# Kernel optimization log

Measured on AMD Instinct MI355X. Metric: run time of the kernel, lower is better.

Reference implementation:

```python
import jax, jax.numpy as jnp
import numpy as np

NUM_HEADS = 4

def setup_inputs() -> dict:
    key = jax.random.key(0)
    ks = jax.random.split(key, 8)
    B, C, H, W = 4, 256, 128, 128
    Cq = C // 8  # query/key channels
    x  = jax.random.normal(ks[0], (B, C, H, W), dtype=jnp.float32)
    Wq = jax.random.normal(ks[1], (Cq, C), dtype=jnp.float32) * 0.05
    bq = jax.random.normal(ks[2], (Cq,),  dtype=jnp.float32) * 0.01
    Wk = jax.random.normal(ks[3], (Cq, C), dtype=jnp.float32) * 0.05
    bk = jax.random.normal(ks[4], (Cq,),  dtype=jnp.float32) * 0.01
    Wv = jax.random.normal(ks[5], (C, C),  dtype=jnp.float32) * 0.05
    bv = jax.random.normal(ks[6], (C,),   dtype=jnp.float32) * 0.01
    # torch init is zeros; use a nonzero value so the attention path contributes
    gamma = jnp.array([0.5], dtype=jnp.float32)
    return {"x": x, "Wq": Wq, "bq": bq, "Wk": Wk, "bk": bk, "Wv": Wv, "bv": bv, "gamma": gamma}

def _conv1x1(x, Wm, b):
    # 1x1 conv == per-pixel linear map over channels
    return jnp.einsum('bchw,oc->bohw', x, Wm) + b[None, :, None, None]

def reference(x, Wq, bq, Wk, bk, Wv, bv, gamma):
    B, C, H, W = x.shape
    nh = NUM_HEADS
    # project, then fold heads into batch: (B*nh, c_head, H, W)
    q = _conv1x1(x, Wq, bq).reshape(B * nh, -1, H, W)
    k = _conv1x1(x, Wk, bk).reshape(B * nh, -1, H, W)
    v = _conv1x1(x, Wv, bv).reshape(B * nh, -1, H, W)
    # horizontal (row-wise) attention over W: energy [BH, H, W, W]
    e_h = jnp.einsum('bchw,bchv->bhwv', q, k)
    a_h = jax.nn.softmax(e_h, axis=-1)
    o_h = jnp.einsum('bhwv,bchv->bchw', a_h, v)  # (BH, cv, H, W)
    # vertical (column-wise) attention over H: energy [BH, W, H, H]
    e_v = jnp.einsum('bchw,bcgw->bwhg', q, k)
    a_v = jax.nn.softmax(e_v, axis=-1)
    # original permutes back as (BH, cv, W, H); requires H == W to add
    o_v = jnp.einsum('bwhg,bcgw->bcwh', a_v, v)
    attn = (o_h + o_v).reshape(B, C, H, W)
    return gamma * attn + x
```

## Files before the change

### kernel.cpp

```cpp
#include <hip/hip_runtime.h>

#define HW 16384

typedef __attribute__((ext_vector_type(8))) short short8;
typedef __attribute__((ext_vector_type(16))) float floatx16;

__device__ inline unsigned short f2bf(float f) {
    unsigned u = __builtin_bit_cast(unsigned, f);
    u = (u + 0x7FFFu + ((u >> 16) & 1u)) >> 16;
    return (unsigned short)u;
}

__device__ inline unsigned pack_bf_trunc(float lo, float hi) {
    return __builtin_amdgcn_perm(__builtin_bit_cast(unsigned, hi),
                                 __builtin_bit_cast(unsigned, lo), 0x07060302u);
}

__global__ __launch_bounds__(256) void castW_kernel(
    const float* __restrict__ Wq, const float* __restrict__ Wk,
    const float* __restrict__ Wv, unsigned short* __restrict__ Wb)
{
    int idx4 = blockIdx.x * 256 + threadIdx.x;
    int e0 = idx4 * 4;
    int row = e0 >> 8, col = e0 & 255;
    const float* src = (row < 32) ? (Wq + row * 256 + col)
                     : (row < 64) ? (Wk + (row - 32) * 256 + col)
                                  : (Wv + (row - 64) * 256 + col);
    float4 v = *(const float4*)src;
    uint2 pk;
    pk.x = f2bf(v.x) | ((unsigned)f2bf(v.y) << 16);
    pk.y = f2bf(v.z) | ((unsigned)f2bf(v.w) << 16);
    *(uint2*)&Wb[e0] = pk;
}

__global__ __launch_bounds__(256) void cast_xt_kernel(
    const float* __restrict__ x, unsigned short* __restrict__ xt)
{
    __shared__ unsigned short T[64][66];
    const int tid = threadIdx.x;
    const int p0 = blockIdx.x * 64;
    const int c0 = blockIdx.y * 64;
    const int b  = blockIdx.z;
    #pragma unroll
    for (int i = 0; i < 4; i++) {
        int e = i * 256 + tid;
        int c = e >> 4, seg = e & 15;
        float4 v = *(const float4*)&x[((b * 256 + c0 + c) << 14) + p0 + seg * 4];
        ((unsigned*)&T[c][seg * 4])[0] = f2bf(v.x) | ((unsigned)f2bf(v.y) << 16);
        ((unsigned*)&T[c][seg * 4])[1] = f2bf(v.z) | ((unsigned)f2bf(v.w) << 16);
    }
    __syncthreads();
    #pragma unroll
    for (int i = 0; i < 2; i++) {
        int e = i * 256 + tid;
        int p = e >> 3, cs = e & 7;
        unsigned short t[8];
        #pragma unroll
        for (int j = 0; j < 8; j++) t[j] = T[cs * 8 + j][p];
        uint4 pk;
        pk.x = t[0] | ((unsigned)t[1] << 16);
        pk.y = t[2] | ((unsigned)t[3] << 16);
        pk.z = t[4] | ((unsigned)t[5] << 16);
        pk.w = t[6] | ((unsigned)t[7] << 16);
        *(uint4*)&xt[(((b << 14) + p0 + p) << 8) + c0 + cs * 8] = pk;
    }
}

__global__ __launch_bounds__(256, 3) void proj_mfma_kernel(
    const unsigned short* __restrict__ Wb, const unsigned short* __restrict__ xt,
    const float* __restrict__ bq, const float* __restrict__ bk,
    const float* __restrict__ bv,
    unsigned short* __restrict__ qb, unsigned short* __restrict__ kb,
    unsigned short* __restrict__ vb)
{
    __shared__ __align__(16) unsigned short As[64 * 64];
    __shared__ __align__(16) unsigned short Bs[256 * 64];
    __shared__ float biasS[64];
    const int tid = threadIdx.x;
    const int p0  = blockIdx.x * 256;
    const int oc0 = blockIdx.y * 64;
    const int b   = blockIdx.z;
    const int w = tid >> 6, lr = tid & 31, lh = (tid & 63) >> 5;

    if (tid < 64) biasS[tid] = (oc0 == 0) ? ((tid < 32) ? bq[tid] : bk[tid - 32])
                                          : bv[oc0 - 64 + tid];

    floatx16 z16 = {0,0,0,0,0,0,0,0,0,0,0,0,0,0,0,0};
    floatx16 acc[2][2] = {{z16, z16}, {z16, z16}};
    const int bpx = (b << 14) + p0;

    for (int kc = 0; kc < 256; kc += 64) {
        if (kc) __syncthreads();
        #pragma unroll
        for (int i = 0; i < 2; i++) {
            int e = i * 256 + tid;
            int row = e >> 3, seg = e & 7, cp = seg ^ (row & 7);
            *(uint4*)&As[row * 64 + cp * 8] =
                *(const uint4*)&Wb[(oc0 + row) * 256 + kc + seg * 8];
        }
        #pragma unroll
        for (int i = 0; i < 8; i++) {
            int e = i * 256 + tid;
            int row = e >> 3, seg = e & 7, cp = seg ^ (row & 7);
            *(uint4*)&Bs[row * 64 + cp * 8] =
                *(const uint4*)&xt[((bpx + row) << 8) + kc + seg * 8];
        }
        __syncthreads();
        #pragma unroll
        for (int ks = 0; ks < 4; ks++) {
            int c = 2 * ks + lh;
            int cx = (c ^ (lr & 7)) * 8;
            short8 af0 = *(const short8*)&As[lr * 64 + cx];
            short8 af1 = *(const short8*)&As[(32 + lr) * 64 + cx];
            short8 bf0 = *(const short8*)&Bs[(64 * w + lr) * 64 + cx];
            short8 bf1 = *(const short8*)&Bs[(64 * w + 32 + lr) * 64 + cx];
            acc[0][0] = __builtin_amdgcn_mfma_f32_32x32x16_bf16(af0, bf0, acc[0][0], 0, 0, 0);
            acc[0][1] = __builtin_amdgcn_mfma_f32_32x32x16_bf16(af0, bf1, acc[0][1], 0, 0, 0);
            acc[1][0] = __builtin_amdgcn_mfma_f32_32x32x16_bf16(af1, bf0, acc[1][0], 0, 0, 0);
            acc[1][1] = __builtin_amdgcn_mfma_f32_32x32x16_bf16(af1, bf1, acc[1][1], 0, 0, 0);
        }
    }

    __syncthreads();
    if (oc0 == 0) {
        unsigned short* Cq = Bs;
        #pragma unroll
        for (int i = 0; i < 2; i++) {
            #pragma unroll
            for (int j = 0; j < 2; j++) {
                int px = 64 * w + 32 * j + lr;
                #pragma unroll
                for (int g = 0; g < 4; g++) {
                    float v0 = acc[i][j][4*g+0] + biasS[32*i + 8*g + 4*lh + 0];
                    float v1 = acc[i][j][4*g+1] + biasS[32*i + 8*g + 4*lh + 1];
                    float v2 = acc[i][j][4*g+2] + biasS[32*i + 8*g + 4*lh + 2];
                    float v3 = acc[i][j][4*g+3] + biasS[32*i + 8*g + 4*lh + 3];
                    uint2 u; u.x = pack_bf_trunc(v0, v1); u.y = pack_bf_trunc(v2, v3);
                    int cp = (4 * i + g) ^ (px & 7);
                    *(uint2*)&Cq[px * 64 + cp * 8 + 4 * lh] = u;
                }
            }
        }
        __syncthreads();
        #pragma unroll
        for (int i = 0; i < 8; i++) {
            int px = tid;
            int cp = i ^ (px & 7);
            uint4 val = *(const uint4*)&Cq[px * 64 + cp * 8];
            if (i < 4) *(uint4*)&qb[(unsigned)((b * 4 + i)     * HW + p0 + px) * 8] = val;
            else       *(uint4*)&kb[(unsigned)((b * 4 + i - 4) * HW + p0 + px) * 8] = val;
        }
    } else {
        unsigned short* Cv = Bs;
        #pragma unroll
        for (int i = 0; i < 2; i++) {
            #pragma unroll
            for (int j = 0; j < 2; j++) {
                int px = 64 * w + 32 * j + lr;
                #pragma unroll
                for (int reg = 0; reg < 16; reg++) {
                    int oc = 32 * i + (reg & 3) + 8 * (reg >> 2) + 4 * lh;
                    float v = acc[i][j][reg] + biasS[oc];
                    int cp = (px >> 3) ^ (oc & 31);
                    Cv[oc * 256 + cp * 8 + (px & 7)] =
                        (unsigned short)(__builtin_bit_cast(unsigned, v) >> 16);
                }
            }
        }
        __syncthreads();
        #pragma unroll
        for (int i = 0; i < 8; i++) {
            int u = i * 256 + tid;
            int oc = u >> 5, seg = u & 31;
            int cp = seg ^ (oc & 31);
            uint4 val = *(const uint4*)&Cv[oc * 256 + cp * 8];
            *(uint4*)&vb[(unsigned)(b * 256 + oc0 - 64 + oc) * HW + p0 + seg * 8] = val;
        }
    }
}

__global__ __launch_bounds__(256) void tqk_kernel(
    const unsigned short* __restrict__ qb, const unsigned short* __restrict__ kb,
    unsigned short* __restrict__ qt, unsigned short* __restrict__ kt)
{
    __shared__ uint4 t[32][33];
    const int plane = blockIdx.y;
    const int tile  = blockIdx.x;
    const int tx = tile & 3, ty = tile >> 2;
    const uint4* src = (const uint4*)(plane < 16 ? qb : kb) + (plane & 15) * HW;
    uint4*       dst = (uint4*)(plane < 16 ? qt : kt) + (plane & 15) * HW;
    const int c = threadIdx.x & 31, r0 = threadIdx.x >> 5;
    #pragma unroll
    for (int i = 0; i < 4; i++) {
        int r = r0 + i * 8;
        t[r][c] = src[(ty * 32 + r) * 128 + tx * 32 + c];
    }
    __syncthreads();
    #pragma unroll
    for (int i = 0; i < 4; i++) {
        int r = r0 + i * 8;
        dst[(tx * 32 + r) * 128 + ty * 32 + c] = t[c][r];
    }
}

__global__ __launch_bounds__(256) void tv_kernel(
    const unsigned short* __restrict__ vb, unsigned short* __restrict__ vt)
{
    __shared__ unsigned short T[64][66];
    const int plane = blockIdx.y;
    const int tile  = blockIdx.x;
    const int tx = tile & 1, ty = tile >> 1;
    const unsigned* src = (const unsigned*)(vb + plane * HW);
    unsigned*       dst = (unsigned*)(vt + plane * HW);
    const int tid = threadIdx.x;
    #pragma unroll
    for (int i = 0; i < 8; i++) {
        int e = i * 256 + tid;
        int r = e >> 5, cp = e & 31;
        *(unsigned*)&T[r][2 * cp] = src[(ty * 64 + r) * 64 + tx * 32 + cp];
    }
    __syncthreads();
    #pragma unroll
    for (int i = 0; i < 8; i++) {
        int e = i * 256 + tid;
        int c = e >> 5, rp = e & 31;
        unsigned lo = T[2 * rp][c], hi = T[2 * rp + 1][c];
        dst[(tx * 64 + c) * 64 + ty * 32 + rp] = lo | (hi << 16);
    }
}

__global__ __launch_bounds__(256, 3) void attn_kernel(
    const unsigned short* __restrict__ qb, const unsigned short* __restrict__ kb,
    const unsigned short* __restrict__ vb,
    const unsigned short* __restrict__ qt, const unsigned short* __restrict__ kt,
    const unsigned short* __restrict__ vt,
    const float* __restrict__ xin, const float* __restrict__ gamma,
    float* __restrict__ out)
{
    __shared__ __align__(16) unsigned short Vs[64 * 128];
    __shared__ __align__(16) unsigned short Ps[128 * 128];
    __shared__ float red[4][128];

    const int tid = threadIdx.x;
    const int y = blockIdx.x, bh = blockIdx.y;
    const int w = tid >> 6, l = tid & 63, lr = l & 31, lh = l >> 5;
    const float L2E = 1.4426950408889634f;

    floatx16 z16 = {0,0,0,0,0,0,0,0,0,0,0,0,0,0,0,0};
    floatx16 o0 = z16, o1 = z16;
    short8 z8 = {0,0,0,0,0,0,0,0};

    for (int stage = 0; stage < 2; stage++) {
        const unsigned short* qsrc = (stage ? qt : qb) + (bh * 128 + y) * 1024;
        const unsigned short* ksrc = (stage ? kt : kb) + (bh * 128 + y) * 1024;
        const unsigned short* vsrc = stage ? vt : vb;
        if (stage) __syncthreads();
        #pragma unroll
        for (int i = 0; i < 4; i++) {
            int e = i * 256 + tid;
            int ch = e >> 4, sg = e & 15;
            int sgp = sg ^ (ch & 15);
            *(uint4*)&Vs[ch * 128 + sgp * 8] =
                *(const uint4*)(vsrc + (bh * 64 + ch) * HW + y * 128 + sg * 8);
        }
        short8 af = z8;
        short8 bf[4] = {z8, z8, z8, z8};
        if (lh == 0) {
            af = *(const short8*)(ksrc + (32 * w + lr) * 8);
            #pragma unroll
            for (int nt = 0; nt < 4; nt++)
                bf[nt] = *(const short8*)(qsrc + (32 * nt + lr) * 8);
        }
        floatx16 et[4];
        #pragma unroll
        for (int nt = 0; nt < 4; nt++)
            et[nt] = __builtin_amdgcn_mfma_f32_32x32x16_bf16(af, bf[nt], z16, 0, 0, 0);

        #pragma unroll
        for (int nt = 0; nt < 4; nt++) {
            float s = 0.f;
            #pragma unroll
            for (int r = 0; r < 16; r++) {
                float p = exp2f(et[nt][r] * L2E);
                et[nt][r] = p;
                s += p;
            }
            s += __shfl_xor(s, 32);
            if (lh == 0) red[w][32 * nt + lr] = s;
        }
        __syncthreads();
        float rl[4];
        #pragma unroll
        for (int nt = 0; nt < 4; nt++) {
            int q = 32 * nt + lr;
            rl[nt] = 1.0f / (red[0][q] + red[1][q] + red[2][q] + red[3][q]);
        }
        #pragma unroll
        for (int nt = 0; nt < 4; nt++) {
            int row = 32 * nt + lr;
            #pragma unroll
            for (int g = 0; g < 4; g++) {
                uint2 u;
                u.x = pack_bf_trunc(et[nt][4*g+0] * rl[nt], et[nt][4*g+1] * rl[nt]);
                u.y = pack_bf_trunc(et[nt][4*g+2] * rl[nt], et[nt][4*g+3] * rl[nt]);
                int cp = (4 * w + g) ^ (lr & 15);
                *(uint2*)&Ps[row * 128 + cp * 8 + 4 * lh] = u;
            }
        }
        __syncthreads();
        #pragma unroll
        for (int ks = 0; ks < 8; ks++) {
            int cp = ((2 * ks + lh) ^ (lr & 15)) * 8;
            short8 pf = *(const short8*)&Ps[(32 * w + lr) * 128 + cp];
            short8 v0 = *(const short8*)&Vs[lr * 128 + cp];
            short8 v1 = *(const short8*)&Vs[(32 + lr) * 128 + cp];
            o0 = __builtin_amdgcn_mfma_f32_32x32x16_bf16(v0, pf, o0, 0, 0, 0);
            o1 = __builtin_amdgcn_mfma_f32_32x32x16_bf16(v1, pf, o1, 0, 0, 0);
        }
    }

    const float g = gamma[0];
    const int xq = 32 * w + lr;
    #pragma unroll
    for (int reg = 0; reg < 16; reg++) {
        int ch = (reg & 3) + 8 * (reg >> 2) + 4 * lh;
        int idx0 = (bh * 64 + ch) * HW + y * 128 + xq;
        int idx1 = (bh * 64 + 32 + ch) * HW + y * 128 + xq;
        out[idx0] = g * o0[reg] + xin[idx0];
        out[idx1] = g * o1[reg] + xin[idx1];
    }
}

extern "C" void kernel_launch(void* const* d_in, const int* in_sizes, int n_in,
                              void* d_out, int out_size, void* d_ws, size_t ws_size,
                              hipStream_t stream) {
    const float* x     = (const float*)d_in[0];
    const float* Wq    = (const float*)d_in[1];
    const float* bq    = (const float*)d_in[2];
    const float* Wk    = (const float*)d_in[3];
    const float* bk    = (const float*)d_in[4];
    const float* Wv    = (const float*)d_in[5];
    const float* bv    = (const float*)d_in[6];
    const float* gamma = (const float*)d_in[7];
    float* out = (float*)d_out;

    unsigned short* Wb   = (unsigned short*)d_ws;
    unsigned short* qb16 = Wb + 320 * 256;
    unsigned short* kb16 = qb16 + 16 * HW * 8;
    unsigned short* qt16 = kb16 + 16 * HW * 8;
    unsigned short* kt16 = qt16 + 16 * HW * 8;
    unsigned short* vb16 = kt16 + 16 * HW * 8;
    unsigned short* vt16 = vb16 + 1024 * HW;
    unsigned short* xt = (unsigned short*)d_out;

    castW_kernel<<<dim3(80), 256, 0, stream>>>(Wq, Wk, Wv, Wb);
    cast_xt_kernel<<<dim3(256, 4, 4), 256, 0, stream>>>(x, xt);
    proj_mfma_kernel<<<dim3(64, 5, 4), 256, 0, stream>>>(Wb, xt, bq, bk, bv, qb16, kb16, vb16);
    tqk_kernel<<<dim3(16, 32), 256, 0, stream>>>(qb16, kb16, qt16, kt16);
    tv_kernel<<<dim3(4, 1024), 256, 0, stream>>>(vb16, vt16);
    attn_kernel<<<dim3(128, 16), 256, 0, stream>>>(qb16, kb16, vb16, qt16, kt16, vt16, x, gamma, out);
}
```

Baseline: 202.4 us.

## Keep softmax probabilities in registers and defer normalization to the epilogue

Each wave now computes energy for its own 32 queries across all 128 keys, so the row sums live inside the wave. This removes the cross-wave shared reduction and the Ps staging buffer in shared memory. Probabilities stay unnormalized in registers and are repacked into MFMA B-operand layout with lane shuffles. The stage-0 accumulator is rescaled by the ratio of the two stages' sums, and the final 1/sum is folded into gamma. Both V tiles are loaded once up front into a double shared buffer, and occupancy hint drops from 3 to 2 blocks, trading occupancy for more registers.

Result: no change. 201.2 us (-0.6%).

```diff
diff --git a/kernel.cpp b/kernel.cpp
--- a/kernel.cpp
+++ b/kernel.cpp
@@ -4,6 +4,7 @@
 
 typedef __attribute__((ext_vector_type(8))) short short8;
 typedef __attribute__((ext_vector_type(16))) float floatx16;
+typedef __attribute__((ext_vector_type(4))) unsigned int uvec4;
 
 __device__ inline unsigned short f2bf(float f) {
     unsigned u = __builtin_bit_cast(unsigned, f);
@@ -229,7 +230,7 @@
     }
 }
 
-__global__ __launch_bounds__(256, 3) void attn_kernel(
+__global__ __launch_bounds__(256, 2) void attn_kernel(
     const unsigned short* __restrict__ qb, const unsigned short* __restrict__ kb,
     const unsigned short* __restrict__ vb,
     const unsigned short* __restrict__ qt, const unsigned short* __restrict__ kt,
@@ -237,97 +238,98 @@
     const float* __restrict__ xin, const float* __restrict__ gamma,
     float* __restrict__ out)
 {
-    __shared__ __align__(16) unsigned short Vs[64 * 128];
-    __shared__ __align__(16) unsigned short Ps[128 * 128];
-    __shared__ float red[4][128];
+    __shared__ __align__(16) unsigned short Vs[2][64 * 128];
 
     const int tid = threadIdx.x;
     const int y = blockIdx.x, bh = blockIdx.y;
     const int w = tid >> 6, l = tid & 63, lr = l & 31, lh = l >> 5;
     const float L2E = 1.4426950408889634f;
 
+    #pragma unroll
+    for (int s = 0; s < 2; s++) {
+        const unsigned short* vsrc = s ? vt : vb;
+        #pragma unroll
+        for (int i = 0; i < 4; i++) {
+            int e = i * 256 + tid;
+            int ch = e >> 4, sg = e & 15, sgp = sg ^ (ch & 15);
+            *(uint4*)&Vs[s][ch * 128 + sgp * 8] =
+                *(const uint4*)(vsrc + (bh * 64 + ch) * HW + y * 128 + sg * 8);
+        }
+    }
+    __syncthreads();
+
     floatx16 z16 = {0,0,0,0,0,0,0,0,0,0,0,0,0,0,0,0};
     floatx16 o0 = z16, o1 = z16;
     short8 z8 = {0,0,0,0,0,0,0,0};
-
+    float s0s = 1.0f;
+
+    #pragma unroll
     for (int stage = 0; stage < 2; stage++) {
         const unsigned short* qsrc = (stage ? qt : qb) + (bh * 128 + y) * 1024;
         const unsigned short* ksrc = (stage ? kt : kb) + (bh * 128 + y) * 1024;
-        const unsigned short* vsrc = stage ? vt : vb;
-        if (stage) __syncthreads();
-        #pragma unroll
-        for (int i = 0; i < 4; i++) {
-            int e = i * 256 + tid;
-            int ch = e >> 4, sg = e & 15;
-            int sgp = sg ^ (ch & 15);
-            *(uint4*)&Vs[ch * 128 + sgp * 8] =
-                *(const uint4*)(vsrc + (bh * 64 + ch) * HW + y * 128 + sg * 8);
-        }
-        short8 af = z8;
-        short8 bf[4] = {z8, z8, z8, z8};
-        if (lh == 0) {
-            af = *(const short8*)(ksrc + (32 * w + lr) * 8);
-            #pragma unroll
-            for (int nt = 0; nt < 4; nt++)
-                bf[nt] = *(const short8*)(qsrc + (32 * nt + lr) * 8);
-        }
-        floatx16 et[4];
-        #pragma unroll
-        for (int nt = 0; nt < 4; nt++)
-            et[nt] = __builtin_amdgcn_mfma_f32_32x32x16_bf16(af, bf[nt], z16, 0, 0, 0);
-
-        #pragma unroll
-        for (int nt = 0; nt < 4; nt++) {
-            float s = 0.f;
+        short8 bf = z8;
+        if (lh == 0) bf = *(const short8*)(qsrc + (32 * w + lr) * 8);
+
+        float partial = 0.f;
+        short8 pf[8];
+        #pragma unroll
+        for (int kg = 0; kg < 4; kg++) {
+            short8 af = z8;
+            if (lh == 0) af = *(const short8*)(ksrc + (32 * kg + lr) * 8);
+            floatx16 e = __builtin_amdgcn_mfma_f32_32x32x16_bf16(af, bf, z16, 0, 0, 0);
             #pragma unroll
             for (int r = 0; r < 16; r++) {
-                float p = exp2f(et[nt][r] * L2E);
-                et[nt][r] = p;
-                s += p;
+                float p = exp2f(e[r] * L2E);
+                e[r] = p;
+                partial += p;
             }
-            s += __shfl_xor(s, 32);
-            if (lh == 0) red[w][32 * nt + lr] = s;
-        }
-        __syncthreads();
-        float rl[4];
-        #pragma unroll
-        for (int nt = 0; nt < 4; nt++) {
-            int q = 32 * nt + lr;
-            rl[nt] = 1.0f / (red[0][q] + red[1][q] + red[2][q] + red[3][q]);
-        }
-        #pragma unroll
-        for (int nt = 0; nt < 4; nt++) {
-            int row = 32 * nt + lr;
-            #pragma unroll
-            for (int g = 0; g < 4; g++) {
-                uint2 u;
-                u.x = pack_bf_trunc(et[nt][4*g+0] * rl[nt], et[nt][4*g+1] * rl[nt]);
-                u.y = pack_bf_trunc(et[nt][4*g+2] * rl[nt], et[nt][4*g+3] * rl[nt]);
-                int cp = (4 * w + g) ^ (lr & 15);
-                *(uint2*)&Ps[row * 128 + cp * 8 + 4 * lh] = u;
+            #pragma unroll
+            for (int cc = 0; cc < 2; cc++) {
+                unsigned X0 = pack_bf_trunc(e[8*cc+0], e[8*cc+1]);
+                unsigned X1 = pack_bf_trunc(e[8*cc+2], e[8*cc+3]);
+                unsigned X2 = pack_bf_trunc(e[8*cc+4], e[8*cc+5]);
+                unsigned X3 = pack_bf_trunc(e[8*cc+6], e[8*cc+7]);
+                unsigned pX0 = __shfl_xor(X0, 32);
+                unsigned pX1 = __shfl_xor(X1, 32);
+                unsigned pX2 = __shfl_xor(X2, 32);
+                unsigned pX3 = __shfl_xor(X3, 32);
+                uvec4 t;
+                t.x = lh ? pX2 : X0;
+                t.y = lh ? pX3 : X1;
+                t.z = lh ? X2  : pX0;
+                t.w = lh ? X3  : pX1;
+                pf[2 * kg + cc] = __builtin_bit_cast(short8, t);
             }
         }
-        __syncthreads();
+        float ssum = partial + __shfl_xor(partial, 32);
+        if (stage == 1) {
+            float f = ssum / s0s;
+            #pragma unroll
+            for (int r = 0; r < 16; r++) { o0[r] *= f; o1[r] *= f; }
+        }
+        s0s = ssum;
+
         #pragma unroll
         for (int ks = 0; ks < 8; ks++) {
             int cp = ((2 * ks + lh) ^ (lr & 15)) * 8;
-            short8 pf = *(const short8*)&Ps[(32 * w + lr) * 128 + cp];
-            short8 v0 = *(const short8*)&Vs[lr * 128 + cp];
-            short8 v1 = *(const short8*)&Vs[(32 + lr) * 128 + cp];
-            o0 = __builtin_amdgcn_mfma_f32_32x32x16_bf16(v0, pf, o0, 0, 0, 0);
-            o1 = __builtin_amdgcn_mfma_f32_32x32x16_bf16(v1, pf, o1, 0, 0, 0);
-        }
-    }
-
-    const float g = gamma[0];
+            short8 v0 = *(const short8*)&Vs[stage][lr * 128 + cp];
+            short8 v1 = *(const short8*)&Vs[stage][(32 + lr) * 128 + cp];
+            o0 = __builtin_amdgcn_mfma_f32_32x32x16_bf16(v0, pf[ks], o0, 0, 0, 0);
+            o1 = __builtin_amdgcn_mfma_f32_32x32x16_bf16(v1, pf[ks], o1, 0, 0, 0);
+        }
+    }
+
+    __syncthreads();
+
+    const float gs = gamma[0] / s0s;
     const int xq = 32 * w + lr;
     #pragma unroll
     for (int reg = 0; reg < 16; reg++) {
         int ch = (reg & 3) + 8 * (reg >> 2) + 4 * lh;
         int idx0 = (bh * 64 + ch) * HW + y * 128 + xq;
         int idx1 = (bh * 64 + 32 + ch) * HW + y * 128 + xq;
-        out[idx0] = g * o0[reg] + xin[idx0];
-        out[idx1] = g * o1[reg] + xin[idx1];
+        out[idx0] = gs * o0[reg] + xin[idx0];
+        out[idx1] = gs * o1[reg] + xin[idx1];
     }
 }
 
```
